# Performance work log

Measured on AMD Instinct MI355X. Metric: run time of the kernel, lower is better.

Reference implementation:

```python
import jax, jax.numpy as jnp
import numpy as np

B_SZ, SEQ, H, P, N, LBLK = 16, 2048, 16, 64, 16, 64  # batch, seqlen, heads, d_head, d_state, block_len


def setup_inputs() -> dict:
    key = jax.random.key(0)
    k1, k2, k3, k4 = jax.random.split(key, 4)
    X = jax.random.normal(k1, (B_SZ, SEQ, H, P), jnp.float32)
    # A is a per-step log-decay; real Mamba2 has A < 0 so exp(segsum) stays bounded
    A = -0.1 * jax.random.uniform(k2, (B_SZ, SEQ, H), jnp.float32)
    B = jax.random.normal(k3, (B_SZ, SEQ, H, N), jnp.float32)
    C = jax.random.normal(k4, (B_SZ, SEQ, H, N), jnp.float32)
    return {"X": X, "A": A, "B": B, "C": C}


def _exp_segsum(x):
    """x: (..., t). Returns exp(cumsum[i]-cumsum[j]) for j<=i, 0 above diagonal."""
    t = x.shape[-1]
    cs = jnp.cumsum(x, axis=-1)
    diff = cs[..., :, None] - cs[..., None, :]
    mask = jnp.tril(jnp.ones((t, t), dtype=bool))
    return jnp.where(mask, jnp.exp(jnp.where(mask, diff, 0.0)), 0.0)


def ssd_forward(X, A, B, C):
    b, s, h, p = X.shape
    n = B.shape[-1]
    c = s // LBLK
    # chunk: (b, c, l, h, *)
    Xb = X.reshape(b, c, LBLK, h, p)
    Bb = B.reshape(b, c, LBLK, h, n)
    Cb = C.reshape(b, c, LBLK, h, n)
    Ab = jnp.transpose(A.reshape(b, c, LBLK, h), (0, 3, 1, 2))  # (b, h, c, l)
    A_cs = jnp.cumsum(Ab, axis=-1)                               # (b, h, c, l)

    # 1. intra-chunk (diagonal block) output: kernel 1
    L = _exp_segsum(Ab)                                          # (b, h, c, l, s)
    CB = jnp.einsum("bclhn,bcshn->bhcls", Cb, Bb)               # (b, h, c, l, s)
    Y_diag = jnp.einsum("bhcls,bcshp->bclhp", CB * L, Xb)

    # 2. per-chunk end states: kernel 2
    decay_states = jnp.exp(A_cs[..., -1:] - A_cs)                # (b, h, c, l)
    states = jnp.einsum("bclhn,bhcl,bclhp->bchpn", Bb, decay_states, Xb)

    # 3. inter-chunk recurrence (zero initial state): kernel 3
    states = jnp.concatenate([jnp.zeros_like(states[:, :1]), states], axis=1)  # (b, c+1, h, p, n)
    A_last_pad = jnp.pad(A_cs[..., -1], ((0, 0), (0, 0), (1, 0)))              # (b, h, c+1)
    decay_chunk = _exp_segsum(A_last_pad)                                       # (b, h, c+1, c+1)
    new_states = jnp.einsum("bhzc,bchpn->bzhpn", decay_chunk, states)
    states_in = new_states[:, :-1]                                              # (b, c, h, p, n)

    # 4. off-diagonal (state -> output) contribution: kernel 4
    Y_off = jnp.einsum("bclhn,bchpn,bhcl->bclhp", Cb, states_in, jnp.exp(A_cs))

    return (Y_diag + Y_off).reshape(b, s, h, p)


def reference(X, A, B, C):
    return ssd_forward(X, A, B, C)
```

## Files before the change

### kernel.cpp

```cpp
#include <hip/hip_runtime.h>

#define BS 16
#define SEQL 2048
#define NH 16
#define PD 64
#define ND 16
#define LB 64
#define NC 32
#define NHP (NH * PD)
#define NHN (NH * ND)

typedef __attribute__((ext_vector_type(8))) short bf16x8;
typedef __attribute__((ext_vector_type(4))) float f32x4;

static __device__ __forceinline__ unsigned short f2bf(float x) {
  unsigned int u = __float_as_uint(x);
  return (unsigned short)((u + 0x7FFFu + ((u >> 16) & 1u)) >> 16);
}
static __device__ __forceinline__ unsigned int pk2(float a, float b) {
  return (unsigned int)f2bf(a) | ((unsigned int)f2bf(b) << 16);
}

static __device__ __forceinline__ void barrier_lds() {
  __builtin_amdgcn_sched_barrier(0);
  asm volatile("s_waitcnt lgkmcnt(0)" ::: "memory");
  __builtin_amdgcn_s_barrier();
  __builtin_amdgcn_sched_barrier(0);
}

static __device__ __forceinline__ int invperm(int l) {
  const int jp = l >> 5, v = l & 31;
  return jp * 32 + (v < 16 ? (((v >> 2) << 3) | (v & 3))
                           : ((((v - 16) >> 2) << 3) | 4 | ((v - 16) & 3)));
}

__global__ __launch_bounds__(512) void ssd_fused(
    const float* __restrict__ Xg, const float* __restrict__ Ag,
    const float* __restrict__ Bg, const float* __restrict__ Cg,
    float* __restrict__ Yg) {
  const int h = blockIdx.x & (NH - 1);
  const int b = blockIdx.x >> 4;
  const int t = threadIdx.x;
  const int w = t >> 6;
  const int lane = t & 63;
  const int g = lane >> 4;
  const int cc = lane & 15;

  __shared__ __align__(16) unsigned short sXt[2][PD][64];
  __shared__ __align__(16) unsigned short sB[2][LB][ND + 8];
  __shared__ __align__(16) unsigned short sC[2][LB][ND + 8];
  __shared__ __align__(16) unsigned short sBdT[2][ND][LB + 8];
  __shared__ __align__(16) float sSTf[2][PD][ND + 4];
  __shared__ __align__(16) unsigned short sSTb[2][PD][ND + 8];
  __shared__ float sER[NC][LB];
  __shared__ float sRR[NC][LB];
  __shared__ float sEtot[NC];

  {
    float av[4];
#pragma unroll
    for (int k = 0; k < 4; ++k)
      av[k] = Ag[((size_t)(b * SEQL + (w + 8 * k) * LB + lane)) * NH + h];
#pragma unroll
    for (int k = 0; k < 4; ++k) {
      const int c = w + 8 * k;
      float v = av[k];
#pragma unroll
      for (int d = 1; d < 64; d <<= 1) {
        float o = __shfl_up(v, d, 64);
        if (lane >= d) v += o;
      }
      const float e = expf(v);
      sER[c][lane] = e;
      sRR[c][lane] = expf(-v);
      if (lane == 63) sEtot[c] = e;
    }
  }
  for (int i = t; i < PD * (ND + 4); i += 512) ((float*)sSTf[0])[i] = 0.f;
  for (int i = t; i < PD * (ND + 8); i += 512) ((unsigned short*)sSTb[0])[i] = 0;
  __syncthreads();

  const int xl0 = (t >> 4) * 2, xp0 = (t & 15) * 4;
  const int bl = t >> 3, bn0 = (t & 7) * 2;
  const int mX = invperm(xl0);
  const int mB = invperm(bl);
  float4 px0, px1;
  float2 pb2, pc2;

#define PREF(ci) do { \
    const size_t s0_ = (size_t)(b * SEQL + (ci) * LB); \
    px0 = *(const float4*)&Xg[(s0_ + xl0) * NHP + h * PD + xp0]; \
    px1 = *(const float4*)&Xg[(s0_ + xl0 + 1) * NHP + h * PD + xp0]; \
    pb2 = *(const float2*)&Bg[(s0_ + bl) * NHN + h * ND + bn0]; \
    pc2 = *(const float2*)&Cg[(s0_ + bl) * NHN + h * ND + bn0]; \
  } while (0)

#define STAGE(bufi, ci) do { \
    _Pragma("unroll") \
    for (int j_ = 0; j_ < 4; ++j_) { \
      const int p_ = xp0 + j_; \
      const int mm_ = ((((mX >> 3) ^ (p_ & 7)) << 3) | (mX & 7)); \
      *(unsigned int*)&sXt[bufi][p_][mm_] = pk2((&px0.x)[j_], (&px1.x)[j_]); \
    } \
    { const float el_ = sER[ci][bl]; \
      const float dl_ = sEtot[ci] * sRR[ci][bl]; \
      *(unsigned int*)&sB[bufi][bl][bn0] = pk2(pb2.x, pb2.y); \
      *(unsigned int*)&sC[bufi][bl][bn0] = pk2(el_ * pc2.x, el_ * pc2.y); \
      sBdT[bufi][bn0][mB] = f2bf(dl_ * pb2.x); \
      sBdT[bufi][bn0 + 1][mB] = f2bf(dl_ * pb2.y); } \
  } while (0)

  const bf16x8 zf8 = {0, 0, 0, 0, 0, 0, 0, 0};
  auto xfrag = [&](int buf, int p_, int kb) -> bf16x8 {
    return *(const bf16x8*)&sXt[buf][p_][(kb ^ (p_ & 7)) << 3];
  };

  PREF(0);
  STAGE(0, 0);
  PREF(1);
  barrier_lds();

  const int lb = w >> 1;
  const int pb0 = (w & 1) * 2;
  const int l = lb * 16 + cc;

  for (int c = 0; c < NC; ++c) {
    const int db = c & 1, nb = db ^ 1;

    bf16x8 cf = zf8;
    if (g < 2) cf = *(const bf16x8*)&sC[db][l][g * 8];
    auto mtile = [&](int sb, bool mask) -> uint2 {
      bf16x8 bfr = zf8;
      if (g < 2) bfr = *(const bf16x8*)&sB[db][sb * 16 + cc][g * 8];
      f32x4 z4 = {0.f, 0.f, 0.f, 0.f};
      f32x4 d = __builtin_amdgcn_mfma_f32_16x16x32_bf16(bfr, cf, z4, 0, 0, 0);
      float m[4];
#pragma unroll
      for (int r = 0; r < 4; ++r) {
        m[r] = d[r] * sRR[c][sb * 16 + 4 * g + r];
        if (mask && (4 * g + r) > cc) m[r] = 0.f;
      }
      return make_uint2(pk2(m[0], m[1]), pk2(m[2], m[3]));
    };
    union { bf16x8 v; unsigned int u[4]; } mf0, mf1;
    mf0.u[0] = mf0.u[1] = mf0.u[2] = mf0.u[3] = 0u;
    mf1.u[0] = mf1.u[1] = mf1.u[2] = mf1.u[3] = 0u;
    if (lb == 0) {
      const uint2 t0 = mtile(0, true);
      mf0.u[0] = t0.x; mf0.u[1] = t0.y;
    } else if (lb == 1) {
      const uint2 t0 = mtile(0, false), t1 = mtile(1, true);
      mf0.u[0] = t0.x; mf0.u[1] = t0.y; mf0.u[2] = t1.x; mf0.u[3] = t1.y;
    } else if (lb == 2) {
      const uint2 t0 = mtile(0, false), t1 = mtile(1, false), t2 = mtile(2, true);
      mf0.u[0] = t0.x; mf0.u[1] = t0.y; mf0.u[2] = t1.x; mf0.u[3] = t1.y;
      mf1.u[0] = t2.x; mf1.u[1] = t2.y;
    } else {
      const uint2 t0 = mtile(0, false), t1 = mtile(1, false);
      const uint2 t2 = mtile(2, false), t3 = mtile(3, true);
      mf0.u[0] = t0.x; mf0.u[1] = t0.y; mf0.u[2] = t1.x; mf0.u[3] = t1.y;
      mf1.u[0] = t2.x; mf1.u[1] = t2.y; mf1.u[2] = t3.x; mf1.u[3] = t3.y;
    }

#pragma unroll
    for (int pbi = 0; pbi < 2; ++pbi) {
      const int p = (pb0 + pbi) * 16 + cc;
      bf16x8 stf = zf8;
      if (g < 2) stf = *(const bf16x8*)&sSTb[db][p][g * 8];
      f32x4 acc = {0.f, 0.f, 0.f, 0.f};
      acc = __builtin_amdgcn_mfma_f32_16x16x32_bf16(cf, stf, acc, 0, 0, 0);
      acc = __builtin_amdgcn_mfma_f32_16x16x32_bf16(mf0.v, xfrag(db, p, g), acc, 0, 0, 0);
      if (lb >= 2)
        acc = __builtin_amdgcn_mfma_f32_16x16x32_bf16(mf1.v, xfrag(db, p, 4 + g), acc, 0, 0, 0);
      const size_t yb =
          ((size_t)(b * SEQL + c * LB + lb * 16 + 4 * g)) * NHP + h * PD + p;
#pragma unroll
      for (int r = 0; r < 4; ++r) Yg[yb + (size_t)r * NHP] = acc[r];
    }

    if (w < 4) {
      const int pS = w * 16 + cc;
      bf16x8 ad0 = *(const bf16x8*)&sBdT[db][cc][g * 8];
      bf16x8 ad1 = *(const bf16x8*)&sBdT[db][cc][32 + g * 8];
      f32x4 s4 = {0.f, 0.f, 0.f, 0.f};
      s4 = __builtin_amdgcn_mfma_f32_16x16x32_bf16(ad0, xfrag(db, pS, g), s4, 0, 0, 0);
      s4 = __builtin_amdgcn_mfma_f32_16x16x32_bf16(ad1, xfrag(db, pS, 4 + g), s4, 0, 0, 0);
      const float etot = sEtot[c];
      float4 old = *(const float4*)&sSTf[db][pS][4 * g];
      float4 nw;
      nw.x = old.x * etot + s4[0];
      nw.y = old.y * etot + s4[1];
      nw.z = old.z * etot + s4[2];
      nw.w = old.w * etot + s4[3];
      *(float4*)&sSTf[nb][pS][4 * g] = nw;
      uint2 ub;
      ub.x = pk2(nw.x, nw.y);
      ub.y = pk2(nw.z, nw.w);
      *(uint2*)&sSTb[nb][pS][4 * g] = ub;
    }

    if (c + 1 < NC) {
      STAGE(nb, c + 1);
      if (c + 2 < NC) PREF(c + 2);
    }
    barrier_lds();
  }
#undef PREF
#undef STAGE
}

extern "C" void kernel_launch(void* const* d_in, const int* in_sizes, int n_in,
                              void* d_out, int out_size, void* d_ws, size_t ws_size,
                              hipStream_t stream) {
  (void)in_sizes; (void)n_in; (void)out_size; (void)d_ws; (void)ws_size;
  const float* X = (const float*)d_in[0];
  const float* A = (const float*)d_in[1];
  const float* B = (const float*)d_in[2];
  const float* C = (const float*)d_in[3];
  float* Y = (float*)d_out;
  ssd_fused<<<BS * NH, 512, 0, stream>>>(X, A, B, C, Y);
}
```

Baseline: 78.40 us.

## Keep running chunk state in registers, redundantly computed per wave

Moves the inter-chunk running state out of shared memory and into per-wave registers. Each of the 8 waves now recomputes the state update for the two p-tiles it consumes, and fragments are rebuilt with lane shuffles. Previously only 4 waves computed the state and wrote fp32 and bf16 copies to LDS. This removes the LDS state buffers, their zero-init, and the store/load round trip. In exchange, the state MFMAs are doubled across waves and shuffle traffic is added every chunk.

```diff
diff --git a/kernel.cpp b/kernel.cpp
--- a/kernel.cpp
+++ b/kernel.cpp
@@ -50,8 +50,6 @@
   __shared__ __align__(16) unsigned short sB[2][LB][ND + 8];
   __shared__ __align__(16) unsigned short sC[2][LB][ND + 8];
   __shared__ __align__(16) unsigned short sBdT[2][ND][LB + 8];
-  __shared__ __align__(16) float sSTf[2][PD][ND + 4];
-  __shared__ __align__(16) unsigned short sSTb[2][PD][ND + 8];
   __shared__ float sER[NC][LB];
   __shared__ float sRR[NC][LB];
   __shared__ float sEtot[NC];
@@ -76,8 +74,6 @@
       if (lane == 63) sEtot[c] = e;
     }
   }
-  for (int i = t; i < PD * (ND + 4); i += 512) ((float*)sSTf[0])[i] = 0.f;
-  for (int i = t; i < PD * (ND + 8); i += 512) ((unsigned short*)sSTb[0])[i] = 0;
   __syncthreads();
 
   const int xl0 = (t >> 4) * 2, xp0 = (t & 15) * 4;
@@ -124,8 +120,34 @@
   const int pb0 = (w & 1) * 2;
   const int l = lb * 16 + cc;
 
+  float stm[2][4];
+#pragma unroll
+  for (int i = 0; i < 2; ++i)
+#pragma unroll
+    for (int r = 0; r < 4; ++r) stm[i][r] = 0.f;
+
   for (int c = 0; c < NC; ++c) {
     const int db = c & 1, nb = db ^ 1;
+
+    bf16x8 stf[2];
+#pragma unroll
+    for (int pbi = 0; pbi < 2; ++pbi) {
+      const unsigned int w0 = pk2(stm[pbi][0], stm[pbi][1]);
+      const unsigned int w1 = pk2(stm[pbi][2], stm[pbi][3]);
+      const unsigned int a0 = __shfl(w0, (lane + 16) & 63, 64);
+      const unsigned int a1 = __shfl(w1, (lane + 16) & 63, 64);
+      const unsigned int b0 = __shfl(w0, (lane + 32) & 63, 64);
+      const unsigned int b1 = __shfl(w1, (lane + 32) & 63, 64);
+      union { bf16x8 v; unsigned int u[4]; } f;
+      if (g == 0) {
+        f.u[0] = w0; f.u[1] = w1; f.u[2] = a0; f.u[3] = a1;
+      } else if (g == 1) {
+        f.u[0] = a0; f.u[1] = a1; f.u[2] = b0; f.u[3] = b1;
+      } else {
+        f.u[0] = 0u; f.u[1] = 0u; f.u[2] = 0u; f.u[3] = 0u;
+      }
+      stf[pbi] = f.v;
+    }
 
     bf16x8 cf = zf8;
     if (g < 2) cf = *(const bf16x8*)&sC[db][l][g * 8];
@@ -165,10 +187,8 @@
 #pragma unroll
     for (int pbi = 0; pbi < 2; ++pbi) {
       const int p = (pb0 + pbi) * 16 + cc;
-      bf16x8 stf = zf8;
-      if (g < 2) stf = *(const bf16x8*)&sSTb[db][p][g * 8];
       f32x4 acc = {0.f, 0.f, 0.f, 0.f};
-      acc = __builtin_amdgcn_mfma_f32_16x16x32_bf16(cf, stf, acc, 0, 0, 0);
+      acc = __builtin_amdgcn_mfma_f32_16x16x32_bf16(cf, stf[pbi], acc, 0, 0, 0);
       acc = __builtin_amdgcn_mfma_f32_16x16x32_bf16(mf0.v, xfrag(db, p, g), acc, 0, 0, 0);
       if (lb >= 2)
         acc = __builtin_amdgcn_mfma_f32_16x16x32_bf16(mf1.v, xfrag(db, p, 4 + g), acc, 0, 0, 0);
@@ -178,25 +198,19 @@
       for (int r = 0; r < 4; ++r) Yg[yb + (size_t)r * NHP] = acc[r];
     }
 
-    if (w < 4) {
-      const int pS = w * 16 + cc;
+    {
       bf16x8 ad0 = *(const bf16x8*)&sBdT[db][cc][g * 8];
       bf16x8 ad1 = *(const bf16x8*)&sBdT[db][cc][32 + g * 8];
-      f32x4 s4 = {0.f, 0.f, 0.f, 0.f};
-      s4 = __builtin_amdgcn_mfma_f32_16x16x32_bf16(ad0, xfrag(db, pS, g), s4, 0, 0, 0);
-      s4 = __builtin_amdgcn_mfma_f32_16x16x32_bf16(ad1, xfrag(db, pS, 4 + g), s4, 0, 0, 0);
       const float etot = sEtot[c];
-      float4 old = *(const float4*)&sSTf[db][pS][4 * g];
-      float4 nw;
-      nw.x = old.x * etot + s4[0];
-      nw.y = old.y * etot + s4[1];
-      nw.z = old.z * etot + s4[2];
-      nw.w = old.w * etot + s4[3];
-      *(float4*)&sSTf[nb][pS][4 * g] = nw;
-      uint2 ub;
-      ub.x = pk2(nw.x, nw.y);
-      ub.y = pk2(nw.z, nw.w);
-      *(uint2*)&sSTb[nb][pS][4 * g] = ub;
+#pragma unroll
+      for (int pbi = 0; pbi < 2; ++pbi) {
+        const int p = (pb0 + pbi) * 16 + cc;
+        f32x4 s4 = {0.f, 0.f, 0.f, 0.f};
+        s4 = __builtin_amdgcn_mfma_f32_16x16x32_bf16(ad0, xfrag(db, p, g), s4, 0, 0, 0);
+        s4 = __builtin_amdgcn_mfma_f32_16x16x32_bf16(ad1, xfrag(db, p, 4 + g), s4, 0, 0, 0);
+#pragma unroll
+        for (int r = 0; r < 4; ++r) stm[pbi][r] = stm[pbi][r] * etot + s4[r];
+      }
     }
 
     if (c + 1 < NC) {
```

Measured after the change: 77.90 us. Within noise of the previous version (-0.6%).
